# Kernel tuning notes

Hardware: AMD Instinct MI355X
Metric: run time of the kernel (lower is better)

The kernel has to match this reference:

```python
import jax, jax.numpy as jnp
import numpy as np

# MxCorrelation (MXNet/FlowNet correlation) parameters
PAD = 4            # pad_size
K = 1              # kernel_size
MAXD = 4           # max_displacement
S1 = 1             # stride1 (output stride)
S2 = 1             # stride2 (displacement stride)


def setup_inputs() -> dict:
    key = jax.random.key(0)
    k1, k2 = jax.random.split(key)
    B, C, H, W = 8, 128, 128, 128
    input1 = jax.random.normal(k1, (B, C, H, W), dtype=jnp.float32)
    input2 = jax.random.normal(k2, (B, C, H, W), dtype=jnp.float32)
    return {"input1": input1, "input2": input2}


def _correlation(a, b):
    # a, b: [B, C, H, W]; returns [B, gw*gw, top_h, top_w]
    B, C, H, W = a.shape
    kr = (K - 1) // 2                       # kernel radius
    border = MAXD + kr                      # border in padded coords
    pa = jnp.pad(a, ((0, 0), (0, 0), (PAD, PAD), (PAD, PAD)))
    pb = jnp.pad(b, ((0, 0), (0, 0), (PAD, PAD), (PAD, PAD)))
    Hp, Wp = H + 2 * PAD, W + 2 * PAD
    th = -(-(Hp - 2 * border) // S1)        # top_height (ceil div)
    tw = -(-(Wp - 2 * border) // S1)        # top_width
    ngr = MAXD // S2                        # neighborhood grid radius
    gw = 2 * ngr + 1                        # grid width -> gw*gw out channels
    sumelems = jnp.float32(K * K * C)       # MXNet normalization

    out = []
    # channel order matches MXNet: row displacement p outer, col q inner
    for p in range(-ngr, ngr + 1):
        for q in range(-ngr, ngr + 1):
            s2p, s2q = p * S2, q * S2
            acc = jnp.zeros((B, th, tw), dtype=a.dtype)
            for dy in range(-kr, kr + 1):
                for dx in range(-kr, kr + 1):
                    A = pa[:, :, border + dy: border + dy + th * S1: S1,
                           border + dx: border + dx + tw * S1: S1]
                    Bm = pb[:, :, border + s2p + dy: border + s2p + dy + th * S1: S1,
                            border + s2q + dx: border + s2q + dx + tw * S1: S1]
                    acc = acc + jnp.sum(A * Bm, axis=1)  # reduce over channels
            out.append(acc / sumelems)
    return jnp.stack(out, axis=1)  # [B, gw*gw, th, tw]


def reference(input1, input2):
    return _correlation(input1, input2)
```

## Files before the change

### kernel.cpp

```cpp
#include <hip/hip_runtime.h>


typedef __fp16 h2 __attribute__((ext_vector_type(2)));

#define BW2 144

#if __has_builtin(__builtin_amdgcn_fdot2)
  #define FDOT2(a, b, c) __builtin_amdgcn_fdot2((a), (b), (c), false)
#else
  static __device__ inline float FDOT2(h2 a, h2 b, float c) {
      return c + (float)a.x * (float)b.x + (float)a.y * (float)b.y;
  }
#endif

static __device__ inline float pk2f(float lo, float hi) {
    h2 v = __builtin_amdgcn_cvt_pkrtz(lo, hi);
    return __builtin_bit_cast(float, v);
}
static __device__ inline h2 f2h2(float f) { return __builtin_bit_cast(h2, f); }

__global__ __launch_bounds__(192, 4)
void corr_kernel(const float* __restrict__ A, const float* __restrict__ B,
                 float* __restrict__ out)
{
    const int bidx = blockIdx.x;
    const int bb = bidx & 7;
    const int t2 = bidx >> 3;
    const int y  = t2 & 127;
    const int pg = t2 >> 7;

    const int tid  = threadIdx.x;
    const int wave = tid >> 6;
    const int lane = tid & 63;
    const int cs   = lane >> 5;
    const int x0   = (lane & 31) << 2;
    const int pr   = pg * 3 + wave;

    __shared__ h2 a_s[2][2][128];
    __shared__ h2 b_s[2][3][2][BW2];

    {
        float4* p = (float4*)&a_s[0][0][0];
        const int na = 2 * 2 * 128 / 4;
        for (int i = tid; i < na; i += 192) p[i] = make_float4(0.f, 0.f, 0.f, 0.f);
        float4* pb = (float4*)&b_s[0][0][0][0];
        const int nb = 2 * 3 * 2 * BW2 / 4;
        for (int i = tid; i < nb; i += 192) pb[i] = make_float4(0.f, 0.f, 0.f, 0.f);
    }

    float acc[9][4];
    #pragma unroll
    for (int q = 0; q < 9; ++q)
        #pragma unroll
        for (int i = 0; i < 4; ++i) acc[q][i] = 0.f;

    const long plane = 128L * 128L;
    const float* Abase = A + (long)bb * 128 * plane + (long)y * 128;
    const float* Bbase = B + (long)bb * 128 * plane;

    const int i4  = (tid & 31) << 2;
    const int rp  = tid >> 5;
    const int brw = rp >> 1;
    const int bpp = rp & 1;
    const int bys = y + pg * 3 + brw - 4;
    const bool bval = (unsigned)bys < 128u;
    const float* Bsrc = Bbase + (long)bys * 128 + i4;

    const bool aact = tid < 64;
    const int app = (tid >> 5) & 1;

    float4 rb0 = make_float4(0.f,0.f,0.f,0.f), rb1 = rb0, ra0 = rb0, ra1 = rb0;

    auto load_chunk = [&](int ch0) {
        if (bval) {
            const int c0 = ch0 + (bpp << 1);
            rb0 = *(const float4*)(Bsrc + (long)c0 * plane);
            rb1 = *(const float4*)(Bsrc + (long)(c0 + 1) * plane);
        }
        if (aact) {
            const int c0 = ch0 + (app << 1);
            ra0 = *(const float4*)(Abase + (long)c0 * plane + i4);
            ra1 = *(const float4*)(Abase + (long)(c0 + 1) * plane + i4);
        }
    };
    auto write_stage = [&](int buf) {
        if (bval) {
            float4 w;
            w.x = pk2f(rb0.x, rb1.x);
            w.y = pk2f(rb0.y, rb1.y);
            w.z = pk2f(rb0.z, rb1.z);
            w.w = pk2f(rb0.w, rb1.w);
            *(float4*)&b_s[buf][brw][bpp][4 + i4] = w;
        }
        if (aact) {
            float4 w;
            w.x = pk2f(ra0.x, ra1.x);
            w.y = pk2f(ra0.y, ra1.y);
            w.z = pk2f(ra0.z, ra1.z);
            w.w = pk2f(ra0.w, ra1.w);
            *(float4*)&a_s[buf][app][i4] = w;
        }
    };

    load_chunk(0);
    __syncthreads();
    write_stage(0);
    load_chunk(4);
    __syncthreads();

    for (int k = 0; k < 32; ++k) {
        const int buf = k & 1;
        if (k + 1 < 32) write_stage(buf ^ 1);
        if (k + 2 < 32) load_chunk((k + 2) << 2);
        {
            const float4 av = *(const float4*)&a_s[buf][cs][x0];
            const float4 b0 = *(const float4*)&b_s[buf][wave][cs][x0];
            const float4 b1 = *(const float4*)&b_s[buf][wave][cs][x0 + 4];
            const float4 b2 = *(const float4*)&b_s[buf][wave][cs][x0 + 8];
            const h2 a2[4] = { f2h2(av.x), f2h2(av.y), f2h2(av.z), f2h2(av.w) };
            const h2 w[12] = { f2h2(b0.x), f2h2(b0.y), f2h2(b0.z), f2h2(b0.w),
                               f2h2(b1.x), f2h2(b1.y), f2h2(b1.z), f2h2(b1.w),
                               f2h2(b2.x), f2h2(b2.y), f2h2(b2.z), f2h2(b2.w) };
            #pragma unroll
            for (int q = 0; q < 9; ++q)
                #pragma unroll
                for (int i = 0; i < 4; ++i)
                    acc[q][i] = FDOT2(a2[i], w[q + i], acc[q][i]);
        }
        __syncthreads();
    }

    #pragma unroll
    for (int q = 0; q < 9; ++q)
        #pragma unroll
        for (int i = 0; i < 4; ++i)
            acc[q][i] += __shfl_down(acc[q][i], 32);

    if (cs == 0) {
        const float scale = 1.0f / 128.0f;
        float* obase = out + (((long)bb * 81 + (long)pr * 9) * 128 + y) * 128 + x0;
        #pragma unroll
        for (int q = 0; q < 9; ++q) {
            const float4 v = make_float4(acc[q][0] * scale, acc[q][1] * scale,
                                         acc[q][2] * scale, acc[q][3] * scale);
            *(float4*)(obase + (long)q * plane) = v;
        }
    }
}

extern "C" void kernel_launch(void* const* d_in, const int* in_sizes, int n_in,
                              void* d_out, int out_size, void* d_ws, size_t ws_size,
                              hipStream_t stream) {
    const float* a = (const float*)d_in[0];
    const float* b = (const float*)d_in[1];
    float* out = (float*)d_out;
    hipLaunchKernelGGL(corr_kernel, dim3(3072), dim3(192), 0, stream, a, b, out);
}
```

Before: 197.5 us.

## Double channel chunk per iteration and deepen register prefetch pipeline

Each loop iteration now processes eight channels instead of four, halving the number of barriers. Global loads are staged through two register sets so data is fetched three chunks ahead. The unused zeroing of the A shared buffer is dropped. This raises register use (16 extra float4s per thread) and doubles shared memory, which may reduce occupancy under the 192x4 launch bounds.

```diff
diff --git a/kernel.cpp b/kernel.cpp
--- a/kernel.cpp
+++ b/kernel.cpp
@@ -36,15 +36,12 @@
     const int x0   = (lane & 31) << 2;
     const int pr   = pg * 3 + wave;
 
-    __shared__ h2 a_s[2][2][128];
-    __shared__ h2 b_s[2][3][2][BW2];
+    __shared__ h2 a_s[2][4][128];
+    __shared__ h2 b_s[2][3][4][BW2];
 
     {
-        float4* p = (float4*)&a_s[0][0][0];
-        const int na = 2 * 2 * 128 / 4;
-        for (int i = tid; i < na; i += 192) p[i] = make_float4(0.f, 0.f, 0.f, 0.f);
         float4* pb = (float4*)&b_s[0][0][0][0];
-        const int nb = 2 * 3 * 2 * BW2 / 4;
+        const int nb = 2 * 3 * 4 * BW2 / 4;
         for (int i = tid; i < nb; i += 192) pb[i] = make_float4(0.f, 0.f, 0.f, 0.f);
     }
 
@@ -61,62 +58,87 @@
     const int i4  = (tid & 31) << 2;
     const int rp  = tid >> 5;
     const int brw = rp >> 1;
-    const int bpp = rp & 1;
+    const int bq  = rp & 1;
     const int bys = y + pg * 3 + brw - 4;
     const bool bval = (unsigned)bys < 128u;
     const float* Bsrc = Bbase + (long)bys * 128 + i4;
 
     const bool aact = tid < 64;
-    const int app = (tid >> 5) & 1;
+    const int aq = (tid >> 5) & 1;
 
-    float4 rb0 = make_float4(0.f,0.f,0.f,0.f), rb1 = rb0, ra0 = rb0, ra1 = rb0;
+    float4 rsb[2][4], rsa[2][4];
+    #pragma unroll
+    for (int s = 0; s < 2; ++s)
+        #pragma unroll
+        for (int i = 0; i < 4; ++i) {
+            rsb[s][i] = make_float4(0.f, 0.f, 0.f, 0.f);
+            rsa[s][i] = make_float4(0.f, 0.f, 0.f, 0.f);
+        }
 
-    auto load_chunk = [&](int ch0) {
+    auto load_chunk = [&](int ch0, int s) {
         if (bval) {
-            const int c0 = ch0 + (bpp << 1);
-            rb0 = *(const float4*)(Bsrc + (long)c0 * plane);
-            rb1 = *(const float4*)(Bsrc + (long)(c0 + 1) * plane);
+            const long c0 = (long)(ch0 + (bq << 1)) * plane;
+            rsb[s][0] = *(const float4*)(Bsrc + c0);
+            rsb[s][1] = *(const float4*)(Bsrc + c0 + plane);
+            rsb[s][2] = *(const float4*)(Bsrc + c0 + 4 * plane);
+            rsb[s][3] = *(const float4*)(Bsrc + c0 + 5 * plane);
         }
         if (aact) {
-            const int c0 = ch0 + (app << 1);
-            ra0 = *(const float4*)(Abase + (long)c0 * plane + i4);
-            ra1 = *(const float4*)(Abase + (long)(c0 + 1) * plane + i4);
+            const long c0 = (long)(ch0 + (aq << 1)) * plane;
+            rsa[s][0] = *(const float4*)(Abase + c0 + i4);
+            rsa[s][1] = *(const float4*)(Abase + c0 + plane + i4);
+            rsa[s][2] = *(const float4*)(Abase + c0 + 4 * plane + i4);
+            rsa[s][3] = *(const float4*)(Abase + c0 + 5 * plane + i4);
         }
     };
-    auto write_stage = [&](int buf) {
+    auto write_stage = [&](int buf, int s) {
         if (bval) {
-            float4 w;
-            w.x = pk2f(rb0.x, rb1.x);
-            w.y = pk2f(rb0.y, rb1.y);
-            w.z = pk2f(rb0.z, rb1.z);
-            w.w = pk2f(rb0.w, rb1.w);
-            *(float4*)&b_s[buf][brw][bpp][4 + i4] = w;
+            float4 w0, w1;
+            w0.x = pk2f(rsb[s][0].x, rsb[s][1].x);
+            w0.y = pk2f(rsb[s][0].y, rsb[s][1].y);
+            w0.z = pk2f(rsb[s][0].z, rsb[s][1].z);
+            w0.w = pk2f(rsb[s][0].w, rsb[s][1].w);
+            w1.x = pk2f(rsb[s][2].x, rsb[s][3].x);
+            w1.y = pk2f(rsb[s][2].y, rsb[s][3].y);
+            w1.z = pk2f(rsb[s][2].z, rsb[s][3].z);
+            w1.w = pk2f(rsb[s][2].w, rsb[s][3].w);
+            *(float4*)&b_s[buf][brw][bq][4 + i4]     = w0;
+            *(float4*)&b_s[buf][brw][bq + 2][4 + i4] = w1;
         }
         if (aact) {
-            float4 w;
-            w.x = pk2f(ra0.x, ra1.x);
-            w.y = pk2f(ra0.y, ra1.y);
-            w.z = pk2f(ra0.z, ra1.z);
-            w.w = pk2f(ra0.w, ra1.w);
-            *(float4*)&a_s[buf][app][i4] = w;
+            float4 w0, w1;
+            w0.x = pk2f(rsa[s][0].x, rsa[s][1].x);
+            w0.y = pk2f(rsa[s][0].y, rsa[s][1].y);
+            w0.z = pk2f(rsa[s][0].z, rsa[s][1].z);
+            w0.w = pk2f(rsa[s][0].w, rsa[s][1].w);
+            w1.x = pk2f(rsa[s][2].x, rsa[s][3].x);
+            w1.y = pk2f(rsa[s][2].y, rsa[s][3].y);
+            w1.z = pk2f(rsa[s][2].z, rsa[s][3].z);
+            w1.w = pk2f(rsa[s][2].w, rsa[s][3].w);
+            *(float4*)&a_s[buf][aq][i4]     = w0;
+            *(float4*)&a_s[buf][aq + 2][i4] = w1;
         }
     };
 
-    load_chunk(0);
+    load_chunk(0, 0);
+    load_chunk(8, 1);
     __syncthreads();
-    write_stage(0);
-    load_chunk(4);
+    write_stage(0, 0);
+    load_chunk(16, 0);
     __syncthreads();
 
-    for (int k = 0; k < 32; ++k) {
+    for (int k = 0; k < 16; ++k) {
         const int buf = k & 1;
-        if (k + 1 < 32) write_stage(buf ^ 1);
-        if (k + 2 < 32) load_chunk((k + 2) << 2);
-        {
-            const float4 av = *(const float4*)&a_s[buf][cs][x0];
-            const float4 b0 = *(const float4*)&b_s[buf][wave][cs][x0];
-            const float4 b1 = *(const float4*)&b_s[buf][wave][cs][x0 + 4];
-            const float4 b2 = *(const float4*)&b_s[buf][wave][cs][x0 + 8];
+        const int ns  = (k + 1) & 1;
+        if (k + 1 < 16) write_stage(ns, ns);
+        if (k + 3 < 16) load_chunk((k + 3) << 3, ns);
+        #pragma unroll
+        for (int pp = 0; pp < 2; ++pp) {
+            const int pa = cs + (pp << 1);
+            const float4 av = *(const float4*)&a_s[buf][pa][x0];
+            const float4 b0 = *(const float4*)&b_s[buf][wave][pa][x0];
+            const float4 b1 = *(const float4*)&b_s[buf][wave][pa][x0 + 4];
+            const float4 b2 = *(const float4*)&b_s[buf][wave][pa][x0 + 8];
             const h2 a2[4] = { f2h2(av.x), f2h2(av.y), f2h2(av.z), f2h2(av.w) };
             const h2 w[12] = { f2h2(b0.x), f2h2(b0.y), f2h2(b0.z), f2h2(b0.w),
                                f2h2(b1.x), f2h2(b1.y), f2h2(b1.z), f2h2(b1.w),
```

Result: slower. 482.1 us (+144.1%).
